# Optimization experiments

Measured on AMD Instinct MI355X. Metric: run time of the kernel, lower is better.

Reference implementation:

```python
import jax, jax.numpy as jnp
import numpy as np

B, N, D, S = 128, 512, 256, 8


def setup_inputs() -> dict:
    key = jax.random.key(0)
    k1, k2, k3, k4, k5, k6, k7 = jax.random.split(key, 7)
    node_feat = jax.random.normal(k1, (B, N, D), dtype=jnp.float32)
    query = jax.random.normal(k2, (B, D), dtype=jnp.float32)
    edge_matrices = jax.random.uniform(k3, (B, N, N), dtype=jnp.float32)
    att_stack = jax.random.uniform(k4, (B, N, S), dtype=jnp.float32)
    # soft one-hot stack pointer (as produced by the controller in the original model)
    ptr_idx = jax.random.randint(k5, (B,), 1, S)
    stack_ptr = jax.nn.one_hot(ptr_idx, S, dtype=jnp.float32)
    value_mem = jnp.zeros((B, N), dtype=jnp.float32)
    W = jax.random.normal(k6, (D, D), dtype=jnp.float32) * 0.02  # nn.Linear weight [out,in]
    b = jnp.zeros((D,), dtype=jnp.float32)
    return {
        "node_feat": node_feat, "query": query, "edge_matrices": edge_matrices,
        "att_stack": att_stack, "stack_ptr": stack_ptr, "value_mem": value_mem,
        "W": W, "b": b,
    }


def reference(node_feat, query, edge_matrices, att_stack, stack_ptr, value_mem, W, b):
    # read_from_stack: weighted sum over stack depth -> key attention [B, N]
    key_attn = jnp.sum(att_stack * stack_ptr[:, None, :], axis=-1)
    # attention-weighted node feature [B, D] and adjacency row [B, N]
    key_feat = jnp.sum(node_feat * key_attn[:, :, None], axis=1)
    edge_matrix = jnp.sum(edge_matrices * key_attn[:, :, None], axis=1)
    # linear projection of key feature -> query vector [B, D]
    q = key_feat @ W.T + b
    # neighbors = node_feat * edge_matrix[..., None]; logits = neighbors @ q
    logits = jnp.einsum('bnd,bn,bd->bn', node_feat, edge_matrix, q)
    # write_to_stack with zero attention: zero out the slot under the pointer
    new_att_stack = att_stack * (1.0 - stack_ptr[:, None, :])
    # _move_ptr_bw: shift pointer toward stack bottom; bottom absorbs itself
    shifted = jnp.concatenate([stack_ptr[:, 1:], jnp.zeros((stack_ptr.shape[0], 1), stack_ptr.dtype)], axis=1)
    new_stack_ptr = shifted.at[:, 0].add(stack_ptr[:, 0])
    new_value_mem = value_mem + logits
    return (new_att_stack, new_stack_ptr, new_value_mem)
```

## Files before the change

### kernel.cpp

```cpp
#include <hip/hip_runtime.h>

#define B 128
#define N 512
#define D 256
#define S 8

__global__ __launch_bounds__(128) void k1_fused(
    const float* __restrict__ node, const float* __restrict__ edge,
    const float* __restrict__ att, const float* __restrict__ spi,
    float* __restrict__ out_att, float* __restrict__ out_sp,
    float* __restrict__ kf, float* __restrict__ em) {
    const int b = blockIdx.y;
    const int role = blockIdx.x;
    const int tid = threadIdx.x;
    __shared__ float sps[S];
    __shared__ float kal[64];
    __shared__ float4 red[64];
    if (tid < S) sps[tid] = spi[b * S + tid];
    __syncthreads();

    if (role < 8) {
        const int i0 = role * 64;
        if (tid < 64) {
            const float4* a = reinterpret_cast<const float4*>(att + ((size_t)(b * N + i0 + tid)) * S);
            float4 a0 = a[0], a1 = a[1];
            kal[tid] = a0.x * sps[0] + a0.y * sps[1] + a0.z * sps[2] + a0.w * sps[3]
                     + a1.x * sps[4] + a1.y * sps[5] + a1.z * sps[6] + a1.w * sps[7];
        }
        __syncthreads();
        float4 acc = make_float4(0.f, 0.f, 0.f, 0.f);
        const float4* base = reinterpret_cast<const float4*>(edge + ((size_t)(b * N + i0)) * N) + tid;
        float4 v[16];
        for (int ii = 0; ii < 64; ii += 16) {
            #pragma unroll
            for (int u = 0; u < 16; ++u) v[u] = base[(size_t)(ii + u) * (N / 4)];
            #pragma unroll
            for (int u = 0; u < 16; ++u) {
                float k = kal[ii + u];
                acc.x += k * v[u].x; acc.y += k * v[u].y;
                acc.z += k * v[u].z; acc.w += k * v[u].w;
            }
        }
        float* dst = em + b * N + tid * 4;
        unsafeAtomicAdd(dst + 0, acc.x);
        unsafeAtomicAdd(dst + 1, acc.y);
        unsafeAtomicAdd(dst + 2, acc.z);
        unsafeAtomicAdd(dst + 3, acc.w);
    } else {
        const int n0 = (role - 8) * 64;
        if (tid < 64) {
            const float4* a = reinterpret_cast<const float4*>(att + ((size_t)(b * N + n0 + tid)) * S);
            float4 a0 = a[0], a1 = a[1];
            kal[tid] = a0.x * sps[0] + a0.y * sps[1] + a0.z * sps[2] + a0.w * sps[3]
                     + a1.x * sps[4] + a1.y * sps[5] + a1.z * sps[6] + a1.w * sps[7];
            float4 o0 = make_float4(a0.x * (1.f - sps[0]), a0.y * (1.f - sps[1]),
                                    a0.z * (1.f - sps[2]), a0.w * (1.f - sps[3]));
            float4 o1 = make_float4(a1.x * (1.f - sps[4]), a1.y * (1.f - sps[5]),
                                    a1.z * (1.f - sps[6]), a1.w * (1.f - sps[7]));
            float4* oa = reinterpret_cast<float4*>(out_att + ((size_t)(b * N + n0 + tid)) * S);
            oa[0] = o0;
            oa[1] = o1;
        }
        if (role == 8 && tid < S) {
            float v = (tid < S - 1) ? sps[tid + 1] : 0.0f;
            if (tid == 0) v += sps[0];
            out_sp[b * S + tid] = v;
        }
        __syncthreads();
        const int col = tid & 63;
        const int r0 = (tid >> 6) * 32;
        float4 acc = make_float4(0.f, 0.f, 0.f, 0.f);
        const float4* base = reinterpret_cast<const float4*>(node + ((size_t)(b * N + n0)) * D) + col;
        float4 v[16];
        for (int ii = 0; ii < 32; ii += 16) {
            #pragma unroll
            for (int u = 0; u < 16; ++u) v[u] = base[(size_t)(r0 + ii + u) * (D / 4)];
            #pragma unroll
            for (int u = 0; u < 16; ++u) {
                float k = kal[r0 + ii + u];
                acc.x += k * v[u].x; acc.y += k * v[u].y;
                acc.z += k * v[u].z; acc.w += k * v[u].w;
            }
        }
        if (tid >= 64) red[col] = acc;
        __syncthreads();
        if (tid < 64) {
            float4 o = red[col];
            acc.x += o.x; acc.y += o.y; acc.z += o.z; acc.w += o.w;
            float* dst = kf + b * D + col * 4;
            unsafeAtomicAdd(dst + 0, acc.x);
            unsafeAtomicAdd(dst + 1, acc.y);
            unsafeAtomicAdd(dst + 2, acc.z);
            unsafeAtomicAdd(dst + 3, acc.w);
        }
    }
}

__global__ void kC_q(const float* __restrict__ Wm,
                     const float* __restrict__ bias,
                     const float* __restrict__ kf,
                     float* __restrict__ q) {
    const int b = blockIdx.x;
    const int d = threadIdx.x;
    __shared__ float kfl[D];
    kfl[d] = kf[b * D + d];
    __syncthreads();
    float acc = bias[d];
    const float4* wrow = reinterpret_cast<const float4*>(Wm + (size_t)d * D);
    const float4* kf4 = reinterpret_cast<const float4*>(kfl);
    float4 w[8];
    for (int k0 = 0; k0 < D / 4; k0 += 8) {
        #pragma unroll
        for (int u = 0; u < 8; ++u) w[u] = wrow[k0 + u];
        #pragma unroll
        for (int u = 0; u < 8; ++u) {
            float4 f = kf4[k0 + u];
            acc += w[u].x * f.x + w[u].y * f.y + w[u].z * f.z + w[u].w * f.w;
        }
    }
    q[b * D + d] = acc;
}

__global__ void kD_logits(const float* __restrict__ node,
                          const float* __restrict__ em,
                          const float* __restrict__ q,
                          const float* __restrict__ vm,
                          float* __restrict__ out_vm) {
    const int row0 = blockIdx.x * 32;
    const int b = row0 / N;
    const int tid = threadIdx.x;
    const int wave = tid >> 6;
    const int lane = tid & 63;
    __shared__ float ql[D];
    if (tid < D) ql[tid] = q[b * D + tid];
    __syncthreads();
    const float4 q4 = reinterpret_cast<const float4*>(ql)[lane];
    const int wr0 = row0 + wave * 8;
    float emv = 0.f, vmv = 0.f;
    if (lane < 8) {
        emv = em[wr0 + lane];
        vmv = vm[wr0 + lane];
    }
    float4 v[8];
    #pragma unroll
    for (int r = 0; r < 8; ++r)
        v[r] = reinterpret_cast<const float4*>(node + (size_t)(wr0 + r) * D)[lane];
    float myS = 0.f;
    #pragma unroll
    for (int r = 0; r < 8; ++r) {
        float s = v[r].x * q4.x + v[r].y * q4.y + v[r].z * q4.z + v[r].w * q4.w;
        #pragma unroll
        for (int off = 32; off; off >>= 1) s += __shfl_xor(s, off);
        if (lane == r) myS = s;
    }
    if (lane < 8) {
        out_vm[wr0 + lane] = vmv + emv * myS;
    }
}

extern "C" void kernel_launch(void* const* d_in, const int* in_sizes, int n_in,
                              void* d_out, int out_size, void* d_ws, size_t ws_size,
                              hipStream_t stream) {
    const float* node = (const float*)d_in[0];
    const float* edge = (const float*)d_in[2];
    const float* att  = (const float*)d_in[3];
    const float* sp   = (const float*)d_in[4];
    const float* vm   = (const float*)d_in[5];
    const float* Wm   = (const float*)d_in[6];
    const float* bias = (const float*)d_in[7];

    float* out_att = (float*)d_out;
    float* out_sp  = out_att + (size_t)B * N * S;
    float* out_vm  = out_sp + (size_t)B * S;

    float* ws = (float*)d_ws;
    float* kf = ws;
    float* em = kf + (size_t)B * D;
    float* q  = em + (size_t)B * N;

    hipMemsetAsync(kf, 0, (size_t)(B * D + B * N) * sizeof(float), stream);

    k1_fused<<<dim3(16, B), 128, 0, stream>>>(node, edge, att, sp,
                                              out_att, out_sp, kf, em);
    kC_q<<<B, D, 0, stream>>>(Wm, bias, kf, q);
    kD_logits<<<(B * N) / 32, 256, 0, stream>>>(node, em, q, vm, out_vm);
}
```

Before: 63.24 us.

## Replace atomic accumulation with per-block partial buffers and drop memset

The first kernel now writes per-block partial sums for the edge row and key feature into separate workspace slices instead of atomically adding into zeroed buffers. Downstream kernels sum the four partials on read, so the memset launch goes away. Blocks are also made larger (256 threads, 128 rows per block, 8 blocks per batch) with in-block shared-memory reduction. This trades atomics and one launch for fewer, larger blocks and slightly more reads in the consumer kernels.

```diff
diff --git a/kernel.cpp b/kernel.cpp
--- a/kernel.cpp
+++ b/kernel.cpp
@@ -5,50 +5,54 @@
 #define D 256
 #define S 8
 
-__global__ __launch_bounds__(128) void k1_fused(
+typedef float f32x4 __attribute__((ext_vector_type(4)));
+
+__global__ __launch_bounds__(256) void k1_fused(
     const float* __restrict__ node, const float* __restrict__ edge,
     const float* __restrict__ att, const float* __restrict__ spi,
     float* __restrict__ out_att, float* __restrict__ out_sp,
-    float* __restrict__ kf, float* __restrict__ em) {
+    float* __restrict__ kf_part, float* __restrict__ em_part) {
     const int b = blockIdx.y;
     const int role = blockIdx.x;
     const int tid = threadIdx.x;
     __shared__ float sps[S];
-    __shared__ float kal[64];
-    __shared__ float4 red[64];
+    __shared__ float kal[128];
+    __shared__ f32x4 red[256];
     if (tid < S) sps[tid] = spi[b * S + tid];
     __syncthreads();
 
-    if (role < 8) {
-        const int i0 = role * 64;
-        if (tid < 64) {
+    if (role < 4) {
+        const int i0 = role * 128;
+        if (tid < 128) {
             const float4* a = reinterpret_cast<const float4*>(att + ((size_t)(b * N + i0 + tid)) * S);
             float4 a0 = a[0], a1 = a[1];
             kal[tid] = a0.x * sps[0] + a0.y * sps[1] + a0.z * sps[2] + a0.w * sps[3]
                      + a1.x * sps[4] + a1.y * sps[5] + a1.z * sps[6] + a1.w * sps[7];
         }
         __syncthreads();
-        float4 acc = make_float4(0.f, 0.f, 0.f, 0.f);
-        const float4* base = reinterpret_cast<const float4*>(edge + ((size_t)(b * N + i0)) * N) + tid;
-        float4 v[16];
-        for (int ii = 0; ii < 64; ii += 16) {
+        const int r = tid >> 7;
+        const int c = tid & 127;
+        const f32x4* base = reinterpret_cast<const f32x4*>(edge + ((size_t)(b * N + i0)) * N)
+                          + (size_t)r * (N / 4) + c;
+        const size_t rs = 2 * (N / 4);
+        f32x4 acc = {0.f, 0.f, 0.f, 0.f};
+        f32x4 v[8];
+        for (int k0 = 0; k0 < 64; k0 += 8) {
             #pragma unroll
-            for (int u = 0; u < 16; ++u) v[u] = base[(size_t)(ii + u) * (N / 4)];
+            for (int u = 0; u < 8; ++u) v[u] = base[(size_t)(k0 + u) * rs];
             #pragma unroll
-            for (int u = 0; u < 16; ++u) {
-                float k = kal[ii + u];
-                acc.x += k * v[u].x; acc.y += k * v[u].y;
-                acc.z += k * v[u].z; acc.w += k * v[u].w;
-            }
+            for (int u = 0; u < 8; ++u) acc += kal[2 * (k0 + u) + r] * v[u];
         }
-        float* dst = em + b * N + tid * 4;
-        unsafeAtomicAdd(dst + 0, acc.x);
-        unsafeAtomicAdd(dst + 1, acc.y);
-        unsafeAtomicAdd(dst + 2, acc.z);
-        unsafeAtomicAdd(dst + 3, acc.w);
+        red[tid] = acc;
+        __syncthreads();
+        if (tid < 128) {
+            f32x4 s = red[tid] + red[tid + 128];
+            reinterpret_cast<f32x4*>(em_part + ((size_t)role * B + b) * N)[tid] = s;
+        }
     } else {
-        const int n0 = (role - 8) * 64;
-        if (tid < 64) {
+        const int p = role - 4;
+        const int n0 = p * 128;
+        if (tid < 128) {
             const float4* a = reinterpret_cast<const float4*>(att + ((size_t)(b * N + n0 + tid)) * S);
             float4 a0 = a[0], a1 = a[1];
             kal[tid] = a0.x * sps[0] + a0.y * sps[1] + a0.z * sps[2] + a0.w * sps[3]
@@ -61,49 +65,46 @@
             oa[0] = o0;
             oa[1] = o1;
         }
-        if (role == 8 && tid < S) {
+        if (p == 0 && tid < S) {
             float v = (tid < S - 1) ? sps[tid + 1] : 0.0f;
             if (tid == 0) v += sps[0];
             out_sp[b * S + tid] = v;
         }
         __syncthreads();
-        const int col = tid & 63;
-        const int r0 = (tid >> 6) * 32;
-        float4 acc = make_float4(0.f, 0.f, 0.f, 0.f);
-        const float4* base = reinterpret_cast<const float4*>(node + ((size_t)(b * N + n0)) * D) + col;
-        float4 v[16];
-        for (int ii = 0; ii < 32; ii += 16) {
+        const int r = tid >> 6;
+        const int c = tid & 63;
+        const f32x4* base = reinterpret_cast<const f32x4*>(node + ((size_t)(b * N + n0)) * D)
+                          + (size_t)r * (D / 4) + c;
+        const size_t rs = 4 * (D / 4);
+        f32x4 acc = {0.f, 0.f, 0.f, 0.f};
+        f32x4 v[8];
+        for (int k0 = 0; k0 < 32; k0 += 8) {
             #pragma unroll
-            for (int u = 0; u < 16; ++u) v[u] = base[(size_t)(r0 + ii + u) * (D / 4)];
+            for (int u = 0; u < 8; ++u) v[u] = base[(size_t)(k0 + u) * rs];
             #pragma unroll
-            for (int u = 0; u < 16; ++u) {
-                float k = kal[r0 + ii + u];
-                acc.x += k * v[u].x; acc.y += k * v[u].y;
-                acc.z += k * v[u].z; acc.w += k * v[u].w;
-            }
+            for (int u = 0; u < 8; ++u) acc += kal[4 * (k0 + u) + r] * v[u];
         }
-        if (tid >= 64) red[col] = acc;
+        red[tid] = acc;
         __syncthreads();
         if (tid < 64) {
-            float4 o = red[col];
-            acc.x += o.x; acc.y += o.y; acc.z += o.z; acc.w += o.w;
-            float* dst = kf + b * D + col * 4;
-            unsafeAtomicAdd(dst + 0, acc.x);
-            unsafeAtomicAdd(dst + 1, acc.y);
-            unsafeAtomicAdd(dst + 2, acc.z);
-            unsafeAtomicAdd(dst + 3, acc.w);
+            f32x4 s = red[c] + red[c + 64] + red[c + 128] + red[c + 192];
+            reinterpret_cast<f32x4*>(kf_part + ((size_t)p * B + b) * D)[c] = s;
         }
     }
 }
 
 __global__ void kC_q(const float* __restrict__ Wm,
                      const float* __restrict__ bias,
-                     const float* __restrict__ kf,
+                     const float* __restrict__ kf_part,
                      float* __restrict__ q) {
     const int b = blockIdx.x;
     const int d = threadIdx.x;
     __shared__ float kfl[D];
-    kfl[d] = kf[b * D + d];
+    float kv = kf_part[(size_t)b * D + d]
+             + kf_part[((size_t)B + b) * D + d]
+             + kf_part[((size_t)2 * B + b) * D + d]
+             + kf_part[((size_t)3 * B + b) * D + d];
+    kfl[d] = kv;
     __syncthreads();
     float acc = bias[d];
     const float4* wrow = reinterpret_cast<const float4*>(Wm + (size_t)d * D);
@@ -122,7 +123,7 @@
 }
 
 __global__ void kD_logits(const float* __restrict__ node,
-                          const float* __restrict__ em,
+                          const float* __restrict__ em_part,
                           const float* __restrict__ q,
                           const float* __restrict__ vm,
                           float* __restrict__ out_vm) {
@@ -138,8 +139,13 @@
     const int wr0 = row0 + wave * 8;
     float emv = 0.f, vmv = 0.f;
     if (lane < 8) {
-        emv = em[wr0 + lane];
-        vmv = vm[wr0 + lane];
+        const int n = wr0 + lane;
+        const int nloc = n - b * N;
+        emv = em_part[(size_t)b * N + nloc]
+            + em_part[((size_t)B + b) * N + nloc]
+            + em_part[((size_t)2 * B + b) * N + nloc]
+            + em_part[((size_t)3 * B + b) * N + nloc];
+        vmv = vm[n];
     }
     float4 v[8];
     #pragma unroll
@@ -174,14 +180,12 @@
     float* out_vm  = out_sp + (size_t)B * S;
 
     float* ws = (float*)d_ws;
-    float* kf = ws;
-    float* em = kf + (size_t)B * D;
-    float* q  = em + (size_t)B * N;
+    float* em_part = ws;
+    float* kf_part = em_part + (size_t)4 * B * N;
+    float* q       = kf_part + (size_t)4 * B * D;
 
-    hipMemsetAsync(kf, 0, (size_t)(B * D + B * N) * sizeof(float), stream);
-
-    k1_fused<<<dim3(16, B), 128, 0, stream>>>(node, edge, att, sp,
-                                              out_att, out_sp, kf, em);
-    kC_q<<<B, D, 0, stream>>>(Wm, bias, kf, q);
-    kD_logits<<<(B * N) / 32, 256, 0, stream>>>(node, em, q, vm, out_vm);
+    k1_fused<<<dim3(8, B), 256, 0, stream>>>(node, edge, att, sp,
+                                             out_att, out_sp, kf_part, em_part);
+    kC_q<<<B, D, 0, stream>>>(Wm, bias, kf_part, q);
+    kD_logits<<<(B * N) / 32, 256, 0, stream>>>(node, em_part, q, vm, out_vm);
 }
```

New measurement: 67.12 us. +6.1%, slower.
